# Optimization experiments

Measured on AMD Instinct MI355X. Metric: run time of the kernel, lower is better.

## Reference

```python
import jax, jax.numpy as jnp
import numpy as np

ANNEAL = 0.01

def _tsig(x, temp=ANNEAL):
    # temperature sigmoid with +/-50 clipping as in the torch source
    return jax.nn.sigmoid(jnp.clip(x / temp, -50.0, 50.0))

def setup_inputs() -> dict:
    key = jax.random.key(0)
    k1, k2 = jax.random.split(key)
    N, D = 512, 512
    preds = jax.random.normal(k1, (N, D), dtype=jnp.float32)
    labels = jax.random.randint(k2, (N,), 0, 64, dtype=jnp.int64)
    return {"preds": preds, "labels": labels}

def reference(preds, labels):
    N = preds.shape[0]
    dtype = preds.dtype
    eye = jnp.eye(N, dtype=dtype)
    same = (labels[:, None] == labels[None, :]).astype(dtype)
    I_pos = same * (1.0 - eye)                      # positives excl. self
    sim_mat = preds @ preds.T                       # [N, N]
    # sim_diff[i, j, k] = sim_mat[i, k] - sim_mat[i, j]
    sim_sg = _tsig(sim_mat[:, None, :] - sim_mat[:, :, None]) * (1.0 - eye)[None, :, :]
    sim_all_rk = 1.0 + jnp.sum(sim_sg, axis=-1)     # [N, N]
    # sum_k sim_sg[i,j,k] * I_pos[i,k]
    pos_sum = jnp.einsum('ijk,ik->ij', sim_sg, I_pos)
    sim_pos_rk = eye + I_pos + I_pos * pos_sum      # [N, N]
    n_pos = jnp.sum(I_pos, axis=1) + 1.0            # [N]
    per_anchor = jnp.sum(sim_pos_rk / sim_all_rk, axis=1) / n_pos
    per_anchor = jnp.where(n_pos > 1.0, per_anchor, 0.0)  # skip anchors with no positives
    ap = jnp.sum(per_anchor) / N
    return 1.0 - ap
```

## Files before the change

### kernel.cpp

```cpp
#include <hip/hip_runtime.h>

#define NN 512
#define NB 256
#define FMAGIC 0x5AD0F1A6u

__global__ __launch_bounds__(512) void sap_fused(const float* __restrict__ P,
                                                 const int* __restrict__ labels,
                                                 unsigned* __restrict__ pa_bits,
                                                 unsigned* __restrict__ flags,
                                                 float* __restrict__ out) {
    __shared__ float srow[2][NN];
    __shared__ int   labels_sh[NN];
    __shared__ float posf[NN];
    __shared__ int   poslist[NN];
    __shared__ int   npos_cnt;
    __shared__ float wave_part[8];
    __shared__ float pa_out[2];
    __shared__ float sh[256];

    const int t    = threadIdx.x;
    const int lane = t & 63;
    const int wave = t >> 6;
    const int g    = lane & 15;
    const int grp  = lane >> 4;
    const int b    = blockIdx.x;
    const int i0   = b * 2;
    const int roff = (b * 37) & (NN - 1);

    if (t < 128) ((int4*)labels_sh)[t] = ((const int4*)labels)[t];

    float4 a0[8], a1[8];
    {
        const float4* A0 = (const float4*)&P[i0 * NN];
        const float4* A1 = (const float4*)&P[(i0 + 1) * NN];
#pragma unroll
        for (int c = 0; c < 8; ++c) {
            a0[c] = A0[g + 16 * c];
            a1[c] = A1[g + 16 * c];
        }
    }

#pragma unroll 4
    for (int bb_ = 0; bb_ < 16; ++bb_) {
        const int k = (wave * 64 + bb_ * 4 + grp + roff) & (NN - 1);
        const float4* B = (const float4*)&P[k * NN];
        float s0 = 0.f, s1 = 0.f;
#pragma unroll
        for (int c = 0; c < 8; ++c) {
            const float4 bb = B[g + 16 * c];
            s0 += a0[c].x * bb.x; s0 += a0[c].y * bb.y;
            s0 += a0[c].z * bb.z; s0 += a0[c].w * bb.w;
            s1 += a1[c].x * bb.x; s1 += a1[c].y * bb.y;
            s1 += a1[c].z * bb.z; s1 += a1[c].w * bb.w;
        }
#pragma unroll
        for (int off = 1; off < 16; off <<= 1) {
            s0 += __shfl_xor(s0, off);
            s1 += __shfl_xor(s1, off);
        }
        if (g == 0) { srow[0][k] = s0; srow[1][k] = s1; }
    }

    const float C1   = 100.0f * 1.44269504088896340736f;
    const float CLIP = 50.0f  * 1.44269504088896340736f;

    for (int a = 0; a < 2; ++a) {
        const int i = i0 + a;
        __syncthreads();
        if (t == 0) npos_cnt = 0;
        if (t < 8) wave_part[t] = 0.f;
        __syncthreads();
        const int li = labels_sh[i];
        {
            bool p  = (labels_sh[t] == li) && (t != i);
            posf[t] = p ? 1.f : 0.f;
            if (p) { int idx = atomicAdd(&npos_cnt, 1); poslist[idx] = t; }
        }
        __syncthreads();

        const int cnt = npos_cnt;
        if (cnt == 0) {
            if (t == 0) pa_out[a] = 0.f;
            continue;
        }

        const float* sr = srow[a];
        float acc = 0.f;
        for (int idx = wave; idx <= cnt; idx += 8) {
            const int   j   = (idx == cnt) ? i : poslist[idx];
            const float sij = sr[j];
            float sum_all = 0.f, sum_pos = 0.f;
#pragma unroll
            for (int kk = 0; kk < 8; kk++) {
                const int k = lane + (kk << 6);
                float y = (sij - sr[k]) * C1;
                y = fminf(fmaxf(y, -CLIP), CLIP);
                float tt = 1.0f / (1.0f + exp2f(y));
                if (k == j) tt = 0.f;
                sum_all += tt;
                sum_pos += tt * posf[k];
            }
#pragma unroll
            for (int off = 32; off; off >>= 1) {
                sum_all += __shfl_down(sum_all, off);
                sum_pos += __shfl_down(sum_pos, off);
            }
            if (lane == 0) {
                const float den = 1.0f + sum_all;
                acc += ((j == i) ? 1.0f : (1.0f + sum_pos)) / den;
            }
        }
        if (lane == 0) wave_part[wave] = acc;
        __syncthreads();
        if (t == 0) {
            float tot = 0.f;
#pragma unroll
            for (int w = 0; w < 8; ++w) tot += wave_part[w];
            pa_out[a] = tot / (float)(cnt + 1);
        }
    }
    __syncthreads();

    if (t == 0) {
        __hip_atomic_store(&pa_bits[i0],     __float_as_uint(pa_out[0]),
                           __ATOMIC_RELAXED, __HIP_MEMORY_SCOPE_AGENT);
        __hip_atomic_store(&pa_bits[i0 + 1], __float_as_uint(pa_out[1]),
                           __ATOMIC_RELAXED, __HIP_MEMORY_SCOPE_AGENT);
        asm volatile("s_waitcnt vmcnt(0)" ::: "memory");
        __hip_atomic_store(&flags[b], FMAGIC,
                           __ATOMIC_RELAXED, __HIP_MEMORY_SCOPE_AGENT);
    }

    if (b != 0) return;

    if (t < NB) {
        while (__hip_atomic_load(&flags[t], __ATOMIC_RELAXED,
                                 __HIP_MEMORY_SCOPE_AGENT) != FMAGIC)
            __builtin_amdgcn_s_sleep(8);
        __hip_atomic_store(&flags[t], 0u, __ATOMIC_RELAXED,
                           __HIP_MEMORY_SCOPE_AGENT);
    }
    __syncthreads();

    if (t < 256) {
        float v0 = __uint_as_float(__hip_atomic_load(&pa_bits[t], __ATOMIC_RELAXED,
                                                     __HIP_MEMORY_SCOPE_AGENT));
        float v1 = __uint_as_float(__hip_atomic_load(&pa_bits[t + 256], __ATOMIC_RELAXED,
                                                     __HIP_MEMORY_SCOPE_AGENT));
        sh[t] = v0 + v1;
    }
    __syncthreads();
    for (int s = 128; s; s >>= 1) {
        if (t < s) sh[t] += sh[t + s];
        __syncthreads();
    }
    if (t == 0) out[0] = 1.0f - sh[0] / (float)NN;
}

extern "C" void kernel_launch(void* const* d_in, const int* in_sizes, int n_in,
                              void* d_out, int out_size, void* d_ws, size_t ws_size,
                              hipStream_t stream) {
    const float* preds  = (const float*)d_in[0];
    const int*   labels = (const int*)d_in[1];
    float* out = (float*)d_out;

    unsigned* pa_bits = (unsigned*)d_ws;
    unsigned* flags   = pa_bits + NN;

    sap_fused<<<NB, 512, 0, stream>>>(preds, labels, pa_bits, flags, out);
}
```

Baseline: 73.07 us.

## Stage anchor rows in LDS and process both anchors concurrently across wave halves

Measured after the change: 73.80 us. No clear change (+1.0%).

```diff
diff --git a/kernel.cpp b/kernel.cpp
--- a/kernel.cpp
+++ b/kernel.cpp
@@ -9,12 +9,13 @@
                                                  unsigned* __restrict__ pa_bits,
                                                  unsigned* __restrict__ flags,
                                                  float* __restrict__ out) {
+    __shared__ float arow[2][NN];
     __shared__ float srow[2][NN];
     __shared__ int   labels_sh[NN];
-    __shared__ float posf[NN];
-    __shared__ int   poslist[NN];
-    __shared__ int   npos_cnt;
-    __shared__ float wave_part[8];
+    __shared__ float posf2[2][NN];
+    __shared__ int   poslist2[2][NN];
+    __shared__ int   npos2[2];
+    __shared__ float wave_part2[2][4];
     __shared__ float pa_out[2];
     __shared__ float sh[256];
 
@@ -25,98 +26,101 @@
     const int grp  = lane >> 4;
     const int b    = blockIdx.x;
     const int i0   = b * 2;
-    const int roff = (b * 37) & (NN - 1);
 
     if (t < 128) ((int4*)labels_sh)[t] = ((const int4*)labels)[t];
+    if (t < 256) ((float4*)&arow[0][0])[t] = ((const float4*)&P[i0 * NN])[t];
+    __syncthreads();
 
-    float4 a0[8], a1[8];
     {
-        const float4* A0 = (const float4*)&P[i0 * NN];
-        const float4* A1 = (const float4*)&P[(i0 + 1) * NN];
+        const float4* A0 = (const float4*)&arow[0][0];
+        const float4* A1 = (const float4*)&arow[1][0];
+#pragma unroll 2
+        for (int bb_ = 0; bb_ < 16; ++bb_) {
+            const int k = wave * 64 + bb_ * 4 + grp;
+            const float4* B = (const float4*)&P[k * NN];
+            float s0 = 0.f, s1 = 0.f;
 #pragma unroll
-        for (int c = 0; c < 8; ++c) {
-            a0[c] = A0[g + 16 * c];
-            a1[c] = A1[g + 16 * c];
+            for (int c = 0; c < 8; ++c) {
+                const float4 bb = B[g + 16 * c];
+                const float4 a0 = A0[g + 16 * c];
+                const float4 a1 = A1[g + 16 * c];
+                s0 += a0.x * bb.x; s0 += a0.y * bb.y;
+                s0 += a0.z * bb.z; s0 += a0.w * bb.w;
+                s1 += a1.x * bb.x; s1 += a1.y * bb.y;
+                s1 += a1.z * bb.z; s1 += a1.w * bb.w;
+            }
+#pragma unroll
+            for (int off = 1; off < 16; off <<= 1) {
+                s0 += __shfl_xor(s0, off);
+                s1 += __shfl_xor(s1, off);
+            }
+            if (g == 0) { srow[0][k] = s0; srow[1][k] = s1; }
         }
-    }
-
-#pragma unroll 4
-    for (int bb_ = 0; bb_ < 16; ++bb_) {
-        const int k = (wave * 64 + bb_ * 4 + grp + roff) & (NN - 1);
-        const float4* B = (const float4*)&P[k * NN];
-        float s0 = 0.f, s1 = 0.f;
-#pragma unroll
-        for (int c = 0; c < 8; ++c) {
-            const float4 bb = B[g + 16 * c];
-            s0 += a0[c].x * bb.x; s0 += a0[c].y * bb.y;
-            s0 += a0[c].z * bb.z; s0 += a0[c].w * bb.w;
-            s1 += a1[c].x * bb.x; s1 += a1[c].y * bb.y;
-            s1 += a1[c].z * bb.z; s1 += a1[c].w * bb.w;
-        }
-#pragma unroll
-        for (int off = 1; off < 16; off <<= 1) {
-            s0 += __shfl_xor(s0, off);
-            s1 += __shfl_xor(s1, off);
-        }
-        if (g == 0) { srow[0][k] = s0; srow[1][k] = s1; }
     }
 
     const float C1   = 100.0f * 1.44269504088896340736f;
     const float CLIP = 50.0f  * 1.44269504088896340736f;
+    const int a  = wave >> 2;
+    const int w4 = wave & 3;
 
-    for (int a = 0; a < 2; ++a) {
-        const int i = i0 + a;
-        __syncthreads();
-        if (t == 0) npos_cnt = 0;
-        if (t < 8) wave_part[t] = 0.f;
-        __syncthreads();
+    __syncthreads();
+    if (t == 0) { npos2[0] = 0; npos2[1] = 0; }
+    if (t < 8) wave_part2[t >> 2][t & 3] = 0.f;
+    __syncthreads();
+#pragma unroll
+    for (int aa = 0; aa < 2; ++aa) {
+        const int i  = i0 + aa;
         const int li = labels_sh[i];
-        {
-            bool p  = (labels_sh[t] == li) && (t != i);
-            posf[t] = p ? 1.f : 0.f;
-            if (p) { int idx = atomicAdd(&npos_cnt, 1); poslist[idx] = t; }
-        }
-        __syncthreads();
+        bool p = (labels_sh[t] == li) && (t != i);
+        posf2[aa][t] = p ? 1.f : 0.f;
+        if (p) { int idx = atomicAdd(&npos2[aa], 1); poslist2[aa][idx] = t; }
+    }
+    __syncthreads();
 
-        const int cnt = npos_cnt;
-        if (cnt == 0) {
-            if (t == 0) pa_out[a] = 0.f;
-            continue;
-        }
-
-        const float* sr = srow[a];
+    {
+        const int   i   = i0 + a;
+        const int   cnt = npos2[a];
         float acc = 0.f;
-        for (int idx = wave; idx <= cnt; idx += 8) {
-            const int   j   = (idx == cnt) ? i : poslist[idx];
-            const float sij = sr[j];
-            float sum_all = 0.f, sum_pos = 0.f;
+        if (cnt > 0) {
+            const float* sr = srow[a];
+            const float* pf = posf2[a];
+            const int*   pl = poslist2[a];
+            for (int idx = w4; idx <= cnt; idx += 4) {
+                const int   j   = (idx == cnt) ? i : pl[idx];
+                const float sij = sr[j];
+                float sum_all = 0.f, sum_pos = 0.f;
 #pragma unroll
-            for (int kk = 0; kk < 8; kk++) {
-                const int k = lane + (kk << 6);
-                float y = (sij - sr[k]) * C1;
-                y = fminf(fmaxf(y, -CLIP), CLIP);
-                float tt = 1.0f / (1.0f + exp2f(y));
-                if (k == j) tt = 0.f;
-                sum_all += tt;
-                sum_pos += tt * posf[k];
-            }
+                for (int kk = 0; kk < 8; kk++) {
+                    const int k = lane + (kk << 6);
+                    float y = (sij - sr[k]) * C1;
+                    y = fminf(fmaxf(y, -CLIP), CLIP);
+                    float tt = 1.0f / (1.0f + exp2f(y));
+                    if (k == j) tt = 0.f;
+                    sum_all += tt;
+                    sum_pos += tt * pf[k];
+                }
 #pragma unroll
-            for (int off = 32; off; off >>= 1) {
-                sum_all += __shfl_down(sum_all, off);
-                sum_pos += __shfl_down(sum_pos, off);
-            }
-            if (lane == 0) {
-                const float den = 1.0f + sum_all;
-                acc += ((j == i) ? 1.0f : (1.0f + sum_pos)) / den;
+                for (int off = 32; off; off >>= 1) {
+                    sum_all += __shfl_down(sum_all, off);
+                    sum_pos += __shfl_down(sum_pos, off);
+                }
+                if (lane == 0) {
+                    const float den = 1.0f + sum_all;
+                    acc += ((j == i) ? 1.0f : (1.0f + sum_pos)) / den;
+                }
             }
         }
-        if (lane == 0) wave_part[wave] = acc;
-        __syncthreads();
-        if (t == 0) {
-            float tot = 0.f;
+        if (lane == 0) wave_part2[a][w4] = acc;
+    }
+    __syncthreads();
+    if (t == 0) {
 #pragma unroll
-            for (int w = 0; w < 8; ++w) tot += wave_part[w];
-            pa_out[a] = tot / (float)(cnt + 1);
+        for (int aa = 0; aa < 2; ++aa) {
+            const int cnt2 = npos2[aa];
+            if (cnt2 == 0) { pa_out[aa] = 0.f; continue; }
+            float tot = wave_part2[aa][0] + wave_part2[aa][1]
+                      + wave_part2[aa][2] + wave_part2[aa][3];
+            pa_out[aa] = tot / (float)(cnt2 + 1);
         }
     }
     __syncthreads();
```

## Double-buffer B rows into LDS with async global_load_lds in dot phase

Applied to the files above, without the earlier changes.

After: 78.61 us. +7.6%, slower.

```diff
diff --git a/kernel.cpp b/kernel.cpp
--- a/kernel.cpp
+++ b/kernel.cpp
@@ -9,6 +9,8 @@
                                                  unsigned* __restrict__ pa_bits,
                                                  unsigned* __restrict__ flags,
                                                  float* __restrict__ out) {
+    __shared__ float stage[8][2][2048];
+    __shared__ float arow[2][NN];
     __shared__ float srow[2][NN];
     __shared__ int   labels_sh[NN];
     __shared__ float posf[NN];
@@ -25,40 +27,62 @@
     const int grp  = lane >> 4;
     const int b    = blockIdx.x;
     const int i0   = b * 2;
-    const int roff = (b * 37) & (NN - 1);
 
     if (t < 128) ((int4*)labels_sh)[t] = ((const int4*)labels)[t];
+    if (t < 256) ((float4*)&arow[0][0])[t] = ((const float4*)&P[i0 * NN])[t];
+    __syncthreads();
 
-    float4 a0[8], a1[8];
     {
-        const float4* A0 = (const float4*)&P[i0 * NN];
-        const float4* A1 = (const float4*)&P[(i0 + 1) * NN];
+        const float4* A0 = (const float4*)&arow[0][0];
+        const float4* A1 = (const float4*)&arow[1][0];
+
+        auto stage_batch = [&](int n, int buf) {
+            const int kbase = wave * 64 + n * 4;
 #pragma unroll
-        for (int c = 0; c < 8; ++c) {
-            a0[c] = A0[g + 16 * c];
-            a1[c] = A1[g + 16 * c];
+            for (int j = 0; j < 8; ++j) {
+                const int r = j >> 1, h = j & 1;
+                const float* gp = &P[(kbase + r) * NN + h * 256 + lane * 4];
+                float* lp = &stage[wave][buf][r * 512 + h * 256];
+                __builtin_amdgcn_global_load_lds(
+                    (const __attribute__((address_space(1))) void*)gp,
+                    (__attribute__((address_space(3))) void*)lp, 16, 0, 0);
+            }
+        };
+        auto dot_batch = [&](int n, int buf) {
+            const int k0 = wave * 64 + n * 4;
+            const float4* B = (const float4*)&stage[wave][buf][grp * 512];
+            float s0 = 0.f, s1 = 0.f;
+#pragma unroll
+            for (int c = 0; c < 8; ++c) {
+                const float4 bb = B[g + 16 * c];
+                const float4 a0 = A0[g + 16 * c];
+                const float4 a1 = A1[g + 16 * c];
+                s0 += a0.x * bb.x; s0 += a0.y * bb.y;
+                s0 += a0.z * bb.z; s0 += a0.w * bb.w;
+                s1 += a1.x * bb.x; s1 += a1.y * bb.y;
+                s1 += a1.z * bb.z; s1 += a1.w * bb.w;
+            }
+#pragma unroll
+            for (int off = 1; off < 16; off <<= 1) {
+                s0 += __shfl_xor(s0, off);
+                s1 += __shfl_xor(s1, off);
+            }
+            if (g == 0) {
+                const int k = k0 + grp;
+                srow[0][k] = s0; srow[1][k] = s1;
+            }
+        };
+
+        stage_batch(0, 0);
+        for (int n = 0; n < 15; ++n) {
+            stage_batch(n + 1, (n + 1) & 1);
+            asm volatile("s_waitcnt vmcnt(8)" ::: "memory");
+            __builtin_amdgcn_sched_barrier(0);
+            dot_batch(n, n & 1);
         }
-    }
-
-#pragma unroll 4
-    for (int bb_ = 0; bb_ < 16; ++bb_) {
-        const int k = (wave * 64 + bb_ * 4 + grp + roff) & (NN - 1);
-        const float4* B = (const float4*)&P[k * NN];
-        float s0 = 0.f, s1 = 0.f;
-#pragma unroll
-        for (int c = 0; c < 8; ++c) {
-            const float4 bb = B[g + 16 * c];
-            s0 += a0[c].x * bb.x; s0 += a0[c].y * bb.y;
-            s0 += a0[c].z * bb.z; s0 += a0[c].w * bb.w;
-            s1 += a1[c].x * bb.x; s1 += a1[c].y * bb.y;
-            s1 += a1[c].z * bb.z; s1 += a1[c].w * bb.w;
-        }
-#pragma unroll
-        for (int off = 1; off < 16; off <<= 1) {
-            s0 += __shfl_xor(s0, off);
-            s1 += __shfl_xor(s1, off);
-        }
-        if (g == 0) { srow[0][k] = s0; srow[1][k] = s1; }
+        asm volatile("s_waitcnt vmcnt(0)" ::: "memory");
+        __builtin_amdgcn_sched_barrier(0);
+        dot_batch(15, 1);
     }
 
     const float C1   = 100.0f * 1.44269504088896340736f;
```
